# Kernel tuning notes

Measured on AMD Instinct MI355X. Metric: run time of the kernel, lower is better.

The kernel has to match this reference:

```python
import jax, jax.numpy as jnp
import numpy as np

N_NODES = 100000
N_EDGES = 1600000
C_IN = 500
HIDDEN = 256
C_OUT = 50
K = 10
K_HALF = K // 2  # 5
ALPHA = 0.1


def _prop(x, src, dst, norm, n):
    # one propagate(): gather source features, scale by edge norm, scatter-add to dst
    msg = norm[:, None] * x[src]          # [E, F]
    return jax.ops.segment_sum(msg, dst, num_segments=n)


def setup_inputs() -> dict:
    key = jax.random.key(0)
    k0, k1, k2, k3 = jax.random.split(key, 4)
    x = jax.random.normal(k0, (N_NODES, C_IN), dtype=jnp.float32)
    edge_index = jax.random.randint(k1, (2, N_EDGES), 0, N_NODES, dtype=jnp.int32)
    # temp[k] = alpha * (1-alpha)^(2k), k = 0..K//2  (even-order PPR coefficients)
    temp = jnp.asarray(ALPHA * (1.0 - ALPHA) ** (2 * np.arange(K_HALF + 1)), dtype=jnp.float32)
    W1 = jax.random.normal(k2, (C_IN, HIDDEN), dtype=jnp.float32) / np.sqrt(C_IN).astype(np.float32)
    b1 = jnp.zeros((HIDDEN,), jnp.float32)
    W2 = jax.random.normal(k3, (HIDDEN, C_OUT), dtype=jnp.float32) / np.sqrt(HIDDEN).astype(np.float32)
    b2 = jnp.zeros((C_OUT,), jnp.float32)
    return {"x": x, "edge_index": edge_index, "W1": W1, "b1": b1, "W2": W2, "b2": b2, "temp": temp}


def reference(x, edge_index, W1, b1, W2, b2, temp):
    n = x.shape[0]
    src, dst = edge_index[0], edge_index[1]
    # sym-normalized adjacency A_hat = D^-1/2 A D^-1/2.
    # (get_laplacian 'sym' then add_self_loops(-norm, 1.0): the -1/+1 diagonal
    #  entries cancel under scatter-add, leaving exactly A_hat.)
    deg = jax.ops.segment_sum(jnp.ones_like(src, dtype=x.dtype), src, num_segments=n)
    dinv = jnp.where(deg > 0, jax.lax.rsqrt(jnp.maximum(deg, 1e-12)), 0.0)
    norm = dinv[src] * dinv[dst]          # [E]

    # MLP (dropout is identity in eval mode)
    h = jax.nn.relu(x @ W1 + b1)
    h = h @ W2 + b2                        # [N, C_OUT]

    hidden0 = h * temp[0]

    def body(k, carry):
        xk, hid = carry
        xk = _prop(xk, src, dst, norm, n)  # A_hat @ x
        xk = _prop(xk, src, dst, norm, n)  # A_hat^2 @ x
        hid = hid + temp[k + 1] * xk
        return (xk, hid)

    _, hidden = jax.lax.fori_loop(0, K_HALF, body, (h, hidden0))
    return jax.nn.log_softmax(hidden, axis=1)
```

## Files before the change

kernel.cpp:

```cpp
#include <hip/hip_runtime.h>

#define NN 100000
#define CIN 500
#define KPAD 512
#define HID 256
#define COUT 50
#define NPADOUT 64

#define NBLK 256
#define CB 128
#define NC ((NN + CB - 1) / CB)
#define NCB (NC * NBLK)
#define NCB2 (2 * NCB)

typedef __attribute__((ext_vector_type(8))) short short8;
typedef __attribute__((ext_vector_type(4))) float f32x4;

static __device__ __forceinline__ unsigned short f2bf(float f) {
  union { float f; unsigned u; } v; v.f = f;
  unsigned r = (v.u + 0x7fffu + ((v.u >> 16) & 1u)) >> 16;
  return (unsigned short)r;
}


__launch_bounds__(256)
__global__ void k_p1(const int* __restrict__ src, const int* __restrict__ dst,
                     int* __restrict__ blk_cnt, int E, int chunk) {
  __shared__ int bd[NC], bs[NC];
  int tid = threadIdx.x;
  for (int i = tid; i < NC; i += 256) { bd[i] = 0; bs[i] = 0; }
  __syncthreads();
  int e0 = blockIdx.x * chunk, e1 = min(E, e0 + chunk);
  for (int e = e0 + tid; e < e1; e += 256) {
    atomicAdd(&bd[dst[e] >> 7], 1);
    atomicAdd(&bs[src[e] >> 7], 1);
  }
  __syncthreads();
  for (int i = tid; i < NC; i += 256) {
    blk_cnt[i * NBLK + blockIdx.x] = bd[i];
    blk_cnt[NCB + i * NBLK + blockIdx.x] = bs[i];
  }
}


__global__ void k_scan_a(const int* __restrict__ hist, int* __restrict__ incl,
                         int* __restrict__ bsum, int n) {
  __shared__ int ts[256];
  int tid = threadIdx.x;
  int base = blockIdx.x * 1024 + tid * 4;
  int a0 = 0, a1 = 0, a2 = 0, a3 = 0;
  if (base + 3 < n) {
    a0 = hist[base]; a1 = hist[base + 1]; a2 = hist[base + 2]; a3 = hist[base + 3];
  } else {
    if (base     < n) a0 = hist[base];
    if (base + 1 < n) a1 = hist[base + 1];
    if (base + 2 < n) a2 = hist[base + 2];
    if (base + 3 < n) a3 = hist[base + 3];
  }
  a1 += a0; a2 += a1; a3 += a2;
  ts[tid] = a3;
  __syncthreads();
  for (int o = 1; o < 256; o <<= 1) {
    int v = ts[tid];
    if (tid >= o) v += ts[tid - o];
    __syncthreads();
    ts[tid] = v;
    __syncthreads();
  }
  int ex = tid ? ts[tid - 1] : 0;
  if (base     < n) incl[base]     = a0 + ex;
  if (base + 1 < n) incl[base + 1] = a1 + ex;
  if (base + 2 < n) incl[base + 2] = a2 + ex;
  if (base + 3 < n) incl[base + 3] = a3 + ex;
  if (tid == 255) bsum[blockIdx.x] = ts[255];
}

__global__ void k_scan_b(const int* __restrict__ bsum, int* __restrict__ bpre, int nb) {
  __shared__ int s[512];
  int tid = threadIdx.x;
  s[tid] = (tid < nb) ? bsum[tid] : 0;
  __syncthreads();
  for (int o = 1; o < 512; o <<= 1) {
    int v = s[tid];
    if (tid >= o) v += s[tid - o];
    __syncthreads();
    s[tid] = v;
    __syncthreads();
  }
  if (tid < nb) bpre[tid] = tid ? s[tid - 1] : 0;
}

__global__ void k_scan_c(const int* __restrict__ incl, const int* __restrict__ bpre,
                         int* __restrict__ slot, int n) {
  int g = blockIdx.x * 256 + threadIdx.x;
  if (g < n) {
    slot[g + 1] = incl[g] + bpre[g >> 10];
    if (g == 0) slot[0] = 0;
  }
}


__launch_bounds__(256)
__global__ void k_p2(const int* __restrict__ src, const int* __restrict__ dst,
                     const int* __restrict__ slot, int* __restrict__ pkd,
                     unsigned char* __restrict__ pks, int E, int chunk) {
  __shared__ int cd[NC], cs[NC];
  int tid = threadIdx.x;
  for (int i = tid; i < NC; i += 256) {
    cd[i] = slot[i * NBLK + blockIdx.x];
    cs[i] = slot[NCB + i * NBLK + blockIdx.x] - E;
  }
  __syncthreads();
  int e0 = blockIdx.x * chunk, e1 = min(E, e0 + chunk);
  for (int e = e0 + tid; e < e1; e += 256) {
    int s = src[e], d = dst[e];
    int pd = atomicAdd(&cd[d >> 7], 1);
    pkd[pd] = (s << 7) | (d & 127);
    int ps = atomicAdd(&cs[s >> 7], 1);
    pks[ps] = (unsigned char)(s & 127);
  }
}


__launch_bounds__(256)
__global__ void k_p3s(const int* __restrict__ slot, const unsigned char* __restrict__ pks,
                      float* __restrict__ dinv, int E) {
  __shared__ int hist[CB];
  int b = blockIdx.x, tid = threadIdx.x;
  if (tid < CB) hist[tid] = 0;
  __syncthreads();
  int s0 = slot[NCB + b * NBLK] - E;
  int s1 = slot[NCB + (b + 1) * NBLK] - E;
  for (int e = s0 + tid; e < s1; e += 256) atomicAdd(&hist[pks[e]], 1);
  __syncthreads();
  if (tid < CB) {
    int node = b * CB + tid;
    if (node < NN) {
      int c = hist[tid];
      dinv[node] = c > 0 ? rsqrtf((float)c) : 0.f;
    }
  }
}


__launch_bounds__(256)
__global__ void k_p3d(const int* __restrict__ slot, const int* __restrict__ pkd,
                      const float* __restrict__ dinv, int* __restrict__ offs,
                      int2* __restrict__ epk, int E) {
  __shared__ int hist[CB], base[CB], cur[CB];
  int b = blockIdx.x, tid = threadIdx.x;
  if (tid < CB) hist[tid] = 0;
  __syncthreads();
  int s0 = slot[b * NBLK];
  int s1 = slot[(b + 1) * NBLK];
  for (int e = s0 + tid; e < s1; e += 256) atomicAdd(&hist[pkd[e] & 127], 1);
  __syncthreads();
  if (tid == 0) {
    int acc = s0;
    for (int i = 0; i < CB; i++) { base[i] = acc; cur[i] = acc; acc += hist[i]; }
  }
  __syncthreads();
  if (tid < CB) {
    int node = b * CB + tid;
    if (node < NN) offs[node] = base[tid];
  }
  if (b == gridDim.x - 1 && tid == 0) offs[NN] = E;
  for (int e = s0 + tid; e < s1; e += 256) {
    int pk = pkd[e];
    int fine = pk & 127, s = pk >> 7;
    int pos = atomicAdd(&cur[fine], 1);
    float nm = dinv[s] * dinv[b * CB + fine];
    epk[pos] = make_int2(s, __float_as_int(nm));
  }
}


__global__ void k_w1t(const float* __restrict__ W1, unsigned short* __restrict__ W1T) {
  int idx = blockIdx.x * 256 + threadIdx.x;
  if (idx < HID * KPAD) {
    int n = idx >> 9, k = idx & 511;
    W1T[idx] = (k < CIN) ? f2bf(W1[(long)k * HID + n]) : (unsigned short)0;
  }
}

__global__ void k_w2t(const float* __restrict__ W2, unsigned short* __restrict__ W2T) {
  int idx = blockIdx.x * 256 + threadIdx.x;
  if (idx < NPADOUT * HID) {
    int n = idx >> 8, k = idx & 255;
    W2T[idx] = (n < COUT) ? f2bf(W2[(long)k * COUT + n]) : (unsigned short)0;
  }
}


__launch_bounds__(512)
__global__ void k_gemm1(const float* __restrict__ X, const unsigned short* __restrict__ W1T,
                        const float* __restrict__ b1, unsigned short* __restrict__ HB) {
  __shared__ unsigned short As[128 * 40];
  __shared__ unsigned short Bs[256 * 40];
  const int tid = threadIdx.x;
  const int lane = tid & 63, w = tid >> 6;
  const int wr = w >> 2, wc = w & 3;
  const int row0 = blockIdx.x * 128;
  f32x4 acc[4][4] = {};
  const int sr = tid >> 3, sc = tid & 7;
  const int br = tid >> 2, bc = tid & 3;

  for (int kk = 0; kk < KPAD; kk += 32) {
    __syncthreads();
#pragma unroll
    for (int p = 0; p < 2; p++) {
      int r = sr + p * 64;
      int grow = row0 + r;
      int gk = kk + sc * 4;
      ushort4 val;
      if (grow < NN && gk < CIN) {
        const float4 f = *reinterpret_cast<const float4*>(&X[(long)grow * CIN + gk]);
        val.x = f2bf(f.x); val.y = f2bf(f.y); val.z = f2bf(f.z); val.w = f2bf(f.w);
      } else {
        val.x = val.y = val.z = val.w = 0;
      }
      *reinterpret_cast<ushort4*>(&As[r * 40 + sc * 4]) = val;
    }
#pragma unroll
    for (int p = 0; p < 2; p++) {
      int nl = br + p * 128;
      const uint4 v = *reinterpret_cast<const uint4*>(&W1T[(long)nl * KPAD + kk + bc * 8]);
      *reinterpret_cast<uint4*>(&Bs[nl * 40 + bc * 8]) = v;
    }
    __syncthreads();
    short8 af[4], bfr[4];
    const int koff = (lane >> 4) * 8;
#pragma unroll
    for (int i = 0; i < 4; i++)
      af[i] = *reinterpret_cast<const short8*>(&As[(wr * 64 + i * 16 + (lane & 15)) * 40 + koff]);
#pragma unroll
    for (int j = 0; j < 4; j++)
      bfr[j] = *reinterpret_cast<const short8*>(&Bs[(wc * 64 + j * 16 + (lane & 15)) * 40 + koff]);
#pragma unroll
    for (int i = 0; i < 4; i++)
#pragma unroll
      for (int j = 0; j < 4; j++)
        acc[i][j] = __builtin_amdgcn_mfma_f32_16x16x32_bf16(af[i], bfr[j], acc[i][j], 0, 0, 0);
  }
#pragma unroll
  for (int i = 0; i < 4; i++) {
    int rbase = row0 + wr * 64 + i * 16 + (lane >> 4) * 4;
#pragma unroll
    for (int j = 0; j < 4; j++) {
      int col = wc * 64 + j * 16 + (lane & 15);
      float bv = b1[col];
#pragma unroll
      for (int r = 0; r < 4; r++) {
        int row = rbase + r;
        if (row < NN) {
          float v = acc[i][j][r] + bv;
          v = v > 0.f ? v : 0.f;
          HB[(long)row * HID + col] = f2bf(v);
        }
      }
    }
  }
}


__launch_bounds__(256)
__global__ void k_gemm2(const unsigned short* __restrict__ HB, const unsigned short* __restrict__ W2T,
                        const float* __restrict__ b2, const float* __restrict__ temp,
                        unsigned short* __restrict__ X0B, float* __restrict__ HIDB) {
  __shared__ unsigned short As[128 * 40];
  __shared__ unsigned short Bs[64 * 40];
  const int tid = threadIdx.x;
  const int lane = tid & 63, w = tid >> 6;
  const int row0 = blockIdx.x * 128;
  f32x4 acc[2][4] = {};
  const int ar = tid >> 2, ac = tid & 3;

  for (int kk = 0; kk < HID; kk += 32) {
    __syncthreads();
#pragma unroll
    for (int p = 0; p < 2; p++) {
      int r = ar + p * 64;
      int grow = row0 + r;
      uint4 v;
      if (grow < NN) v = *reinterpret_cast<const uint4*>(&HB[(long)grow * HID + kk + ac * 8]);
      else { v.x = v.y = v.z = v.w = 0; }
      *reinterpret_cast<uint4*>(&As[r * 40 + ac * 8]) = v;
    }
    {
      int nl = tid >> 2, c = tid & 3;
      const uint4 v = *reinterpret_cast<const uint4*>(&W2T[nl * HID + kk + c * 8]);
      *reinterpret_cast<uint4*>(&Bs[nl * 40 + c * 8]) = v;
    }
    __syncthreads();
    short8 af[2], bfr[4];
    const int koff = (lane >> 4) * 8;
#pragma unroll
    for (int i = 0; i < 2; i++)
      af[i] = *reinterpret_cast<const short8*>(&As[(w * 32 + i * 16 + (lane & 15)) * 40 + koff]);
#pragma unroll
    for (int j = 0; j < 4; j++)
      bfr[j] = *reinterpret_cast<const short8*>(&Bs[(j * 16 + (lane & 15)) * 40 + koff]);
#pragma unroll
    for (int i = 0; i < 2; i++)
#pragma unroll
      for (int j = 0; j < 4; j++)
        acc[i][j] = __builtin_amdgcn_mfma_f32_16x16x32_bf16(af[i], bfr[j], acc[i][j], 0, 0, 0);
  }
  float t0 = temp[0];
#pragma unroll
  for (int i = 0; i < 2; i++) {
    int rbase = row0 + w * 32 + i * 16 + (lane >> 4) * 4;
#pragma unroll
    for (int j = 0; j < 4; j++) {
      int col = j * 16 + (lane & 15);
      if (col < COUT) {
        float bv = b2[col];
#pragma unroll
        for (int r = 0; r < 4; r++) {
          int row = rbase + r;
          if (row < NN) {
            float v = acc[i][j][r] + bv;
            X0B[(long)row * COUT + col] = f2bf(v);
            HIDB[(long)row * COUT + col] = t0 * v;
          }
        }
      }
    }
  }
}


__launch_bounds__(256)
__global__ void k_prop(const int* __restrict__ offs, const int2* __restrict__ epk,
                       const unsigned short* __restrict__ xin,
                       unsigned short* __restrict__ xout, float* __restrict__ hid,
                       const float* __restrict__ temp, int accidx) {
  int node = blockIdx.x * 8 + (threadIdx.x >> 5);
  if (node >= NN) return;
  int h = threadIdx.x & 31;
  int fp = h * 2;
  bool act = fp < COUT;
  int fc = act ? fp : 0;
  int s0 = offs[node], s1 = offs[node + 1];
  float a0 = 0.f, a1 = 0.f;
  int e = s0;
  for (; e + 3 < s1; e += 4) {
    int2 p0 = epk[e], p1 = epk[e + 1], p2 = epk[e + 2], p3 = epk[e + 3];
    unsigned v0 = *reinterpret_cast<const unsigned*>(&xin[(long)p0.x * COUT + fc]);
    unsigned v1 = *reinterpret_cast<const unsigned*>(&xin[(long)p1.x * COUT + fc]);
    unsigned v2 = *reinterpret_cast<const unsigned*>(&xin[(long)p2.x * COUT + fc]);
    unsigned v3 = *reinterpret_cast<const unsigned*>(&xin[(long)p3.x * COUT + fc]);
    float w0 = __int_as_float(p0.y), w1 = __int_as_float(p1.y);
    float w2 = __int_as_float(p2.y), w3 = __int_as_float(p3.y);
    a0 += w0 * __uint_as_float(v0 << 16) + w1 * __uint_as_float(v1 << 16)
        + w2 * __uint_as_float(v2 << 16) + w3 * __uint_as_float(v3 << 16);
    a1 += w0 * __uint_as_float(v0 & 0xffff0000u) + w1 * __uint_as_float(v1 & 0xffff0000u)
        + w2 * __uint_as_float(v2 & 0xffff0000u) + w3 * __uint_as_float(v3 & 0xffff0000u);
  }
  for (; e < s1; e++) {
    int2 p0 = epk[e];
    float w0 = __int_as_float(p0.y);
    unsigned v0 = *reinterpret_cast<const unsigned*>(&xin[(long)p0.x * COUT + fc]);
    a0 += w0 * __uint_as_float(v0 << 16);
    a1 += w0 * __uint_as_float(v0 & 0xffff0000u);
  }
  if (act) {
    unsigned pk = ((unsigned)f2bf(a1) << 16) | (unsigned)f2bf(a0);
    *reinterpret_cast<unsigned*>(&xout[(long)node * COUT + fp]) = pk;
    if (accidx >= 0) {
      float t = temp[accidx];
      float2* hp = reinterpret_cast<float2*>(&hid[(long)node * COUT + fp]);
      float2 o = *hp;
      o.x += t * a0; o.y += t * a1;
      *hp = o;
    }
  }
}


__launch_bounds__(256)
__global__ void k_lsm(const float* __restrict__ hid, float* __restrict__ out) {
  int node = blockIdx.x * 4 + (threadIdx.x >> 6);
  if (node >= NN) return;
  int f = threadIdx.x & 63;
  float v = (f < COUT) ? hid[(long)node * COUT + f] : -INFINITY;
  float m = v;
#pragma unroll
  for (int o = 32; o > 0; o >>= 1) m = fmaxf(m, __shfl_xor(m, o, 64));
  float ex = (f < COUT) ? expf(v - m) : 0.f;
  float s = ex;
#pragma unroll
  for (int o = 32; o > 0; o >>= 1) s += __shfl_xor(s, o, 64);
  if (f < COUT) out[(long)node * COUT + f] = (v - m) - logf(s);
}


extern "C" void kernel_launch(void* const* d_in, const int* in_sizes, int n_in,
                              void* d_out, int out_size, void* d_ws, size_t ws_size,
                              hipStream_t stream) {
  const float* X  = (const float*)d_in[0];
  const int* EI   = (const int*)d_in[1];
  const float* W1 = (const float*)d_in[2];
  const float* B1 = (const float*)d_in[3];
  const float* W2 = (const float*)d_in[4];
  const float* B2 = (const float*)d_in[5];
  const float* TEMP = (const float*)d_in[6];
  const int E = in_sizes[1] / 2;
  const int* src = EI;
  const int* dst = EI + E;

  char* ws = (char*)d_ws;
  size_t off = 0;
  auto alloc = [&](size_t bytes) -> void* {
    off = (off + 511) & ~(size_t)511;
    void* p = ws + off;
    off += bytes;
    return p;
  };
  unsigned short* HB  = (unsigned short*)alloc((size_t)NN * HID * 2);
  unsigned short* W1T = (unsigned short*)alloc((size_t)HID * KPAD * 2);
  unsigned short* W2T = (unsigned short*)alloc((size_t)NPADOUT * HID * 2);
  unsigned short* X0B = (unsigned short*)alloc((size_t)NN * COUT * 2);
  unsigned short* X1B = (unsigned short*)alloc((size_t)NN * COUT * 2);
  float* HIDB = (float*)alloc((size_t)NN * COUT * 4);
  float* DINV = (float*)alloc((size_t)NN * 4);
  int* OFFS   = (int*)alloc((size_t)(NN + 1) * 4);
  int* BLKC   = (int*)alloc((size_t)NCB2 * 4);
  int* INCL   = (int*)alloc((size_t)NCB2 * 4);
  int* SLOT   = (int*)alloc((size_t)(NCB2 + 1) * 4);
  int* BSUM   = (int*)alloc(512 * 4);
  int* BPRE   = (int*)alloc(512 * 4);
  int* PKD    = (int*)alloc((size_t)E * 4);
  unsigned char* PKS = (unsigned char*)alloc((size_t)E);
  int2* EPK   = (int2*)alloc((size_t)E * 8);

  const int chunk = (E + NBLK - 1) / NBLK;
  const int nscan = NCB2;
  const int nsa = (nscan + 1023) / 1024;

  k_p1<<<NBLK, 256, 0, stream>>>(src, dst, BLKC, E, chunk);
  k_scan_a<<<nsa, 256, 0, stream>>>(BLKC, INCL, BSUM, nscan);
  k_scan_b<<<1, 512, 0, stream>>>(BSUM, BPRE, nsa);
  k_scan_c<<<(nscan + 255) / 256, 256, 0, stream>>>(INCL, BPRE, SLOT, nscan);
  k_p2<<<NBLK, 256, 0, stream>>>(src, dst, SLOT, PKD, PKS, E, chunk);
  k_p3s<<<NC, 256, 0, stream>>>(SLOT, PKS, DINV, E);
  k_p3d<<<NC, 256, 0, stream>>>(SLOT, PKD, DINV, OFFS, EPK, E);

  k_w1t<<<(HID * KPAD + 255) / 256, 256, 0, stream>>>(W1, W1T);
  k_w2t<<<(NPADOUT * HID + 255) / 256, 256, 0, stream>>>(W2, W2T);

  k_gemm1<<<(NN + 127) / 128, 512, 0, stream>>>(X, W1T, B1, HB);
  k_gemm2<<<(NN + 127) / 128, 256, 0, stream>>>(HB, W2T, B2, TEMP, X0B, HIDB);

  const int PB = (NN + 7) / 8;
  for (int k = 0; k < 5; k++) {
    k_prop<<<PB, 256, 0, stream>>>(OFFS, EPK, X0B, X1B, HIDB, TEMP, -1);
    k_prop<<<PB, 256, 0, stream>>>(OFFS, EPK, X1B, X0B, HIDB, TEMP, k + 1);
  }
  k_lsm<<<(NN + 3) / 4, 256, 0, stream>>>(HIDB, (float*)d_out);
}
```

Measured before the change: 976.9 us.

## Register-prefetch gemm1 tiles, pad propagation features to 64, merge weight transposes

gemm1 now loads the next K-slice of X and W1T into registers while the MFMAs for the current slice run, which adds a second barrier per iteration. The bf16 propagation buffers get a 64-element row stride so every gather is aligned and index math becomes a shift. The two weight-transpose kernels are merged into one launch. Padding raises the buffer footprint, and the padded columns 50..63 are never written, so they hold uninitialized data that gets loaded but never stored.

```diff
diff --git a/kernel.cpp b/kernel.cpp
--- a/kernel.cpp
+++ b/kernel.cpp
@@ -6,6 +6,7 @@
 #define HID 256
 #define COUT 50
 #define NPADOUT 64
+#define FPAD 64
 
 #define NBLK 256
 #define CB 128
@@ -175,19 +176,16 @@
 }
 
 
-__global__ void k_w1t(const float* __restrict__ W1, unsigned short* __restrict__ W1T) {
+__global__ void k_wt(const float* __restrict__ W1, const float* __restrict__ W2,
+                     unsigned short* __restrict__ W1T, unsigned short* __restrict__ W2T) {
   int idx = blockIdx.x * 256 + threadIdx.x;
   if (idx < HID * KPAD) {
     int n = idx >> 9, k = idx & 511;
     W1T[idx] = (k < CIN) ? f2bf(W1[(long)k * HID + n]) : (unsigned short)0;
-  }
-}
-
-__global__ void k_w2t(const float* __restrict__ W2, unsigned short* __restrict__ W2T) {
-  int idx = blockIdx.x * 256 + threadIdx.x;
-  if (idx < NPADOUT * HID) {
-    int n = idx >> 8, k = idx & 255;
-    W2T[idx] = (n < COUT) ? f2bf(W2[(long)k * COUT + n]) : (unsigned short)0;
+  } else if (idx < HID * KPAD + NPADOUT * HID) {
+    int i2 = idx - HID * KPAD;
+    int n = i2 >> 8, k = i2 & 255;
+    W2T[i2] = (n < COUT) ? f2bf(W2[(long)k * COUT + n]) : (unsigned short)0;
   }
 }
 
@@ -205,27 +203,42 @@
   const int sr = tid >> 3, sc = tid & 7;
   const int br = tid >> 2, bc = tid & 3;
 
-  for (int kk = 0; kk < KPAD; kk += 32) {
-    __syncthreads();
+  float4 ra[2];
+  uint4 rb[2];
+#pragma unroll
+  for (int p = 0; p < 2; p++) {
+    int grow = row0 + sr + p * 64;
+    int gr = grow < NN ? grow : NN - 1;
+    float4 f = *reinterpret_cast<const float4*>(&X[(long)gr * CIN + sc * 4]);
+    if (grow >= NN) { f.x = 0.f; f.y = 0.f; f.z = 0.f; f.w = 0.f; }
+    ra[p] = f;
+    rb[p] = *reinterpret_cast<const uint4*>(&W1T[(long)(br + p * 128) * KPAD + bc * 8]);
+  }
+
+  for (int ks = 0; ks < 16; ks++) {
+    const int kk = ks * 32;
 #pragma unroll
     for (int p = 0; p < 2; p++) {
-      int r = sr + p * 64;
-      int grow = row0 + r;
-      int gk = kk + sc * 4;
       ushort4 val;
-      if (grow < NN && gk < CIN) {
-        const float4 f = *reinterpret_cast<const float4*>(&X[(long)grow * CIN + gk]);
-        val.x = f2bf(f.x); val.y = f2bf(f.y); val.z = f2bf(f.z); val.w = f2bf(f.w);
-      } else {
-        val.x = val.y = val.z = val.w = 0;
+      val.x = f2bf(ra[p].x); val.y = f2bf(ra[p].y);
+      val.z = f2bf(ra[p].z); val.w = f2bf(ra[p].w);
+      *reinterpret_cast<ushort4*>(&As[(sr + p * 64) * 40 + sc * 4]) = val;
+      *reinterpret_cast<uint4*>(&Bs[(br + p * 128) * 40 + bc * 8]) = rb[p];
+    }
+    if (ks < 15) {
+      const int nk = kk + 32;
+      const int gk = nk + sc * 4;
+      const bool kok = gk < CIN;
+      const int gkc = kok ? gk : 0;
+#pragma unroll
+      for (int p = 0; p < 2; p++) {
+        int grow = row0 + sr + p * 64;
+        int gr = grow < NN ? grow : NN - 1;
+        float4 f = *reinterpret_cast<const float4*>(&X[(long)gr * CIN + gkc]);
+        if (grow >= NN || !kok) { f.x = 0.f; f.y = 0.f; f.z = 0.f; f.w = 0.f; }
+        ra[p] = f;
+        rb[p] = *reinterpret_cast<const uint4*>(&W1T[(long)(br + p * 128) * KPAD + nk + bc * 8]);
       }
-      *reinterpret_cast<ushort4*>(&As[r * 40 + sc * 4]) = val;
-    }
-#pragma unroll
-    for (int p = 0; p < 2; p++) {
-      int nl = br + p * 128;
-      const uint4 v = *reinterpret_cast<const uint4*>(&W1T[(long)nl * KPAD + kk + bc * 8]);
-      *reinterpret_cast<uint4*>(&Bs[nl * 40 + bc * 8]) = v;
     }
     __syncthreads();
     short8 af[4], bfr[4];
@@ -241,6 +254,7 @@
 #pragma unroll
       for (int j = 0; j < 4; j++)
         acc[i][j] = __builtin_amdgcn_mfma_f32_16x16x32_bf16(af[i], bfr[j], acc[i][j], 0, 0, 0);
+    __syncthreads();
   }
 #pragma unroll
   for (int i = 0; i < 4; i++) {
@@ -320,7 +334,7 @@
           int row = rbase + r;
           if (row < NN) {
             float v = acc[i][j][r] + bv;
-            X0B[(long)row * COUT + col] = f2bf(v);
+            X0B[((long)row << 6) + col] = f2bf(v);
             HIDB[(long)row * COUT + col] = t0 * v;
           }
         }
@@ -339,17 +353,15 @@
   if (node >= NN) return;
   int h = threadIdx.x & 31;
   int fp = h * 2;
-  bool act = fp < COUT;
-  int fc = act ? fp : 0;
   int s0 = offs[node], s1 = offs[node + 1];
   float a0 = 0.f, a1 = 0.f;
   int e = s0;
   for (; e + 3 < s1; e += 4) {
     int2 p0 = epk[e], p1 = epk[e + 1], p2 = epk[e + 2], p3 = epk[e + 3];
-    unsigned v0 = *reinterpret_cast<const unsigned*>(&xin[(long)p0.x * COUT + fc]);
-    unsigned v1 = *reinterpret_cast<const unsigned*>(&xin[(long)p1.x * COUT + fc]);
-    unsigned v2 = *reinterpret_cast<const unsigned*>(&xin[(long)p2.x * COUT + fc]);
-    unsigned v3 = *reinterpret_cast<const unsigned*>(&xin[(long)p3.x * COUT + fc]);
+    unsigned v0 = *reinterpret_cast<const unsigned*>(&xin[((long)p0.x << 6) + fp]);
+    unsigned v1 = *reinterpret_cast<const unsigned*>(&xin[((long)p1.x << 6) + fp]);
+    unsigned v2 = *reinterpret_cast<const unsigned*>(&xin[((long)p2.x << 6) + fp]);
+    unsigned v3 = *reinterpret_cast<const unsigned*>(&xin[((long)p3.x << 6) + fp]);
     float w0 = __int_as_float(p0.y), w1 = __int_as_float(p1.y);
     float w2 = __int_as_float(p2.y), w3 = __int_as_float(p3.y);
     a0 += w0 * __uint_as_float(v0 << 16) + w1 * __uint_as_float(v1 << 16)
@@ -360,13 +372,13 @@
   for (; e < s1; e++) {
     int2 p0 = epk[e];
     float w0 = __int_as_float(p0.y);
-    unsigned v0 = *reinterpret_cast<const unsigned*>(&xin[(long)p0.x * COUT + fc]);
+    unsigned v0 = *reinterpret_cast<const unsigned*>(&xin[((long)p0.x << 6) + fp]);
     a0 += w0 * __uint_as_float(v0 << 16);
     a1 += w0 * __uint_as_float(v0 & 0xffff0000u);
   }
-  if (act) {
+  if (fp < COUT) {
     unsigned pk = ((unsigned)f2bf(a1) << 16) | (unsigned)f2bf(a0);
-    *reinterpret_cast<unsigned*>(&xout[(long)node * COUT + fp]) = pk;
+    *reinterpret_cast<unsigned*>(&xout[((long)node << 6) + fp]) = pk;
     if (accidx >= 0) {
       float t = temp[accidx];
       float2* hp = reinterpret_cast<float2*>(&hid[(long)node * COUT + fp]);
@@ -420,8 +432,8 @@
   unsigned short* HB  = (unsigned short*)alloc((size_t)NN * HID * 2);
   unsigned short* W1T = (unsigned short*)alloc((size_t)HID * KPAD * 2);
   unsigned short* W2T = (unsigned short*)alloc((size_t)NPADOUT * HID * 2);
-  unsigned short* X0B = (unsigned short*)alloc((size_t)NN * COUT * 2);
-  unsigned short* X1B = (unsigned short*)alloc((size_t)NN * COUT * 2);
+  unsigned short* X0B = (unsigned short*)alloc((size_t)NN * FPAD * 2);
+  unsigned short* X1B = (unsigned short*)alloc((size_t)NN * FPAD * 2);
   float* HIDB = (float*)alloc((size_t)NN * COUT * 4);
   float* DINV = (float*)alloc((size_t)NN * 4);
   int* OFFS   = (int*)alloc((size_t)(NN + 1) * 4);
@@ -446,8 +458,7 @@
   k_p3s<<<NC, 256, 0, stream>>>(SLOT, PKS, DINV, E);
   k_p3d<<<NC, 256, 0, stream>>>(SLOT, PKD, DINV, OFFS, EPK, E);
 
-  k_w1t<<<(HID * KPAD + 255) / 256, 256, 0, stream>>>(W1, W1T);
-  k_w2t<<<(NPADOUT * HID + 255) / 256, 256, 0, stream>>>(W2, W2T);
+  k_wt<<<(HID * KPAD + NPADOUT * HID + 255) / 256, 256, 0, stream>>>(W1, W2, W1T, W2T);
 
   k_gemm1<<<(NN + 127) / 128, 512, 0, stream>>>(X, W1T, B1, HB);
   k_gemm2<<<(NN + 127) / 128, 256, 0, stream>>>(HB, W2T, B2, TEMP, X0B, HIDB);
```

After: 974.1 us. Within noise of the previous version (-0.3%).
